# Kernel optimization log

Measured on AMD Instinct MI355X. Metric: run time of the kernel, lower is better.

## Reference

```python
import jax, jax.numpy as jnp
import numpy as np

N_NODES = 50000
N_EDGES = 800000
IN_C, HID_C, OUT_C = 96, 64, 40
ALPHA = 0.2
K = 2
NEG_SLOPE = 0.01  # F.leaky_relu default


def setup_inputs() -> dict:
    key = jax.random.key(0)
    k_x, k_e, k_w0, k_b0, k_w4, k_b4 = jax.random.split(key, 6)
    x = jax.random.normal(k_x, (N_NODES, IN_C), dtype=jnp.float32)
    edge_index = jax.random.randint(k_e, (2, N_EDGES), 0, N_NODES, dtype=jnp.int64)
    # SGConv linear layers (torch.nn.Linear layout: [out, in])
    W0 = jax.random.normal(k_w0, (HID_C, IN_C), dtype=jnp.float32) / np.sqrt(IN_C)
    b0 = jax.random.normal(k_b0, (HID_C,), dtype=jnp.float32) * 0.01
    W4 = jax.random.normal(k_w4, (OUT_C, HID_C), dtype=jnp.float32) / np.sqrt(HID_C)
    b4 = jax.random.normal(k_b4, (OUT_C,), dtype=jnp.float32) * 0.01
    return {"x": x, "edge_index": edge_index, "W0": W0, "b0": b0, "W4": W4, "b4": b4}


def reference(x, edge_index, W0, b0, W4, b4):
    # GCN normalization with self-loops (shared by SGConv and APPNP in PyG):
    # A_hat = A + I, prop(h) = D^{-1/2} A_hat D^{-1/2} h
    n = x.shape[0]
    loops = jnp.arange(n, dtype=edge_index.dtype)
    src = jnp.concatenate([edge_index[0], loops])
    dst = jnp.concatenate([edge_index[1], loops])
    deg = jax.ops.segment_sum(jnp.ones_like(dst, dtype=x.dtype), dst, num_segments=n)
    dinv = jnp.where(deg > 0, jax.lax.rsqrt(deg), 0.0)
    norm = dinv[src] * dinv[dst]  # [E + N]

    def prop(h):
        # gather -> scale -> scatter-add  (irregular memory-bound core op)
        return jax.ops.segment_sum(norm[:, None] * h[src], dst, num_segments=n)

    def sg_prop(h):  # SGConv: K propagation steps, then linear
        for _ in range(K):
            h = prop(h)
        return h

    def appnp(h0):  # APPNP: z_{k+1} = (1-alpha) * prop(z_k) + alpha * h0
        z = h0
        for _ in range(K):
            z = (1.0 - ALPHA) * prop(z) + ALPHA * h0
        return z

    h = sg_prop(x) @ W0.T + b0          # conv0 (SGConv)
    # dropout is identity in eval mode (training=False)
    h = jax.nn.leaky_relu(appnp(h), NEG_SLOPE)   # conv1
    h = jax.nn.leaky_relu(appnp(h), NEG_SLOPE)   # conv2
    h = jax.nn.leaky_relu(appnp(h), NEG_SLOPE)   # conv3
    h = sg_prop(h) @ W4.T + b4          # conv4 (SGConv)
    return jax.nn.log_softmax(h, axis=1)
```

## Files before the change

kernel.cpp:

```cpp
#include <hip/hip_runtime.h>
#include <hip/hip_fp16.h>
#include <math.h>

#define N_NODES 50000
#define N_EDGES 800000
#define IN_C 96
#define HID_C 64
#define OUT_C 40
#define ALPHA 0.2f
#define NEG_SLOPE 0.01f

typedef _Float16 f16x8 __attribute__((ext_vector_type(8)));
typedef float f32x4 __attribute__((ext_vector_type(4)));

__device__ __forceinline__ int edge_at(const void* ei, int is64, long long pos) {
    return is64 ? (int)((const long long*)ei)[pos] : ((const int*)ei)[pos];
}

__global__ void zero_detect_k(int* deg, int n, const unsigned int* ei, int* flag) {
    int i = blockIdx.x * blockDim.x + threadIdx.x;
    if (i < n) deg[i] = 0;
    if (i == 0) {
        int is64 = 1;
        for (int j = 1; j < 16; j += 2)
            if (ei[j] != 0u) is64 = 0;
        *flag = is64;
    }
}

__global__ void deg_hist_k(const void* ei, const int* flag, int* deg, int E) {
    int e = blockIdx.x * blockDim.x + threadIdx.x;
    if (e < E) {
        int d = edge_at(ei, *flag, (long long)E + e);
        atomicAdd(&deg[d], 1);
    }
}

__global__ void scan_p1_k(const int* __restrict__ deg, int* __restrict__ part, int n) {
    __shared__ int sm[256];
    int t = threadIdx.x, i = blockIdx.x * 256 + t;
    int v = (i < n) ? deg[i] : 0;
    sm[t] = v;
    __syncthreads();
    for (int off = 1; off < 256; off <<= 1) {
        int u = (t >= off) ? sm[t - off] : 0;
        __syncthreads();
        sm[t] += u;
        __syncthreads();
    }
    if (t == 255) part[blockIdx.x] = sm[255];
}

__global__ void scan_p2_k(int* part, int nb, int* rowptr, int n) {
    __shared__ int sm[256];
    int t = threadIdx.x;
    int v = (t < nb) ? part[t] : 0;
    sm[t] = v;
    __syncthreads();
    for (int off = 1; off < 256; off <<= 1) {
        int u = (t >= off) ? sm[t - off] : 0;
        __syncthreads();
        sm[t] += u;
        __syncthreads();
    }
    if (t < nb) part[t] = sm[t] - v;
    if (t == 255) rowptr[n] = sm[255];
}

__global__ void scan_p3_k(const int* __restrict__ deg, const int* __restrict__ part,
                          int* __restrict__ rowptr, int* __restrict__ cursor,
                          float* __restrict__ dinv, int n) {
    __shared__ int sm[256];
    int t = threadIdx.x, i = blockIdx.x * 256 + t;
    int v = (i < n) ? deg[i] : 0;
    sm[t] = v;
    __syncthreads();
    for (int off = 1; off < 256; off <<= 1) {
        int u = (t >= off) ? sm[t - off] : 0;
        __syncthreads();
        sm[t] += u;
        __syncthreads();
    }
    if (i < n) {
        int excl = sm[t] - v + part[blockIdx.x];
        rowptr[i] = excl;
        cursor[i] = excl;
        dinv[i] = rsqrtf((float)v + 1.0f);
    }
}

#define FILL_CHUNK 8192
__global__ void csr_fill_k(const void* ei, const int* flag,
                           int* __restrict__ cursor, int* __restrict__ csrc,
                           int E, int N) {
    int p = blockIdx.x & 7;
    int chunk = blockIdx.x >> 3;
    int lo = p * (N / 8), hi = lo + (N / 8);
    int e0 = chunk * FILL_CHUNK;
    int e1 = e0 + FILL_CHUNK; if (e1 > E) e1 = E;
    int f = *flag;
    for (int e = e0 + threadIdx.x; e < e1; e += blockDim.x) {
        int d = edge_at(ei, f, (long long)E + e);
        if (d >= lo && d < hi) {
            int s = edge_at(ei, f, e);
            int pos = atomicAdd(&cursor[d], 1);
            csrc[pos] = s;
        }
    }
}

template <bool COMBINE, bool LEAKY, bool BIAS>
__global__ void prop64_k(const int* __restrict__ rowptr, const int* __restrict__ csrc,
                         const float* __restrict__ dinv,
                         const __half* __restrict__ in, const __half* __restrict__ h0,
                         const float* __restrict__ bias,
                         __half* __restrict__ out, int N) {
    int node = blockIdx.x * (blockDim.x >> 4) + (threadIdx.x >> 4);
    int ci = threadIdx.x & 15;
    if (node >= N) return;
    const float2* in4 = (const float2*)in;
    f32x4 acc;
    {
        float2 r = in4[node * 16 + ci];
        float2 a = __half22float2(*(const __half2*)&r.x);
        float2 b = __half22float2(*(const __half2*)&r.y);
        acc[0] = a.x; acc[1] = a.y; acc[2] = b.x; acc[3] = b.y;
    }
    int r0 = rowptr[node], r1 = rowptr[node + 1];
    int i = r0;
    for (; i + 3 < r1; i += 4) {
        int s0 = csrc[i], s1 = csrc[i + 1], s2 = csrc[i + 2], s3 = csrc[i + 3];
        float2 v0 = in4[s0 * 16 + ci];
        float2 v1 = in4[s1 * 16 + ci];
        float2 v2 = in4[s2 * 16 + ci];
        float2 v3 = in4[s3 * 16 + ci];
        float2 a0 = __half22float2(*(const __half2*)&v0.x), b0 = __half22float2(*(const __half2*)&v0.y);
        float2 a1 = __half22float2(*(const __half2*)&v1.x), b1 = __half22float2(*(const __half2*)&v1.y);
        float2 a2 = __half22float2(*(const __half2*)&v2.x), b2 = __half22float2(*(const __half2*)&v2.y);
        float2 a3 = __half22float2(*(const __half2*)&v3.x), b3 = __half22float2(*(const __half2*)&v3.y);
        acc[0] += (a0.x + a1.x) + (a2.x + a3.x);
        acc[1] += (a0.y + a1.y) + (a2.y + a3.y);
        acc[2] += (b0.x + b1.x) + (b2.x + b3.x);
        acc[3] += (b0.y + b1.y) + (b2.y + b3.y);
    }
    for (; i < r1; ++i) {
        float2 v0 = in4[csrc[i] * 16 + ci];
        float2 a0 = __half22float2(*(const __half2*)&v0.x), b0 = __half22float2(*(const __half2*)&v0.y);
        acc[0] += a0.x; acc[1] += a0.y; acc[2] += b0.x; acc[3] += b0.y;
    }
    float di = dinv[node];
    float sc = di * di;
    float4 v;
    v.x = sc * acc[0]; v.y = sc * acc[1]; v.z = sc * acc[2]; v.w = sc * acc[3];
    if (BIAS) {
        const float4 b = ((const float4*)bias)[ci];
        v.x += di * b.x; v.y += di * b.y; v.z += di * b.z; v.w += di * b.w;
    }
    if (COMBINE) {
        float2 r = ((const float2*)h0)[node * 16 + ci];
        float2 a = __half22float2(*(const __half2*)&r.x);
        float2 b = __half22float2(*(const __half2*)&r.y);
        v.x = (1.0f - ALPHA) * v.x + ALPHA * a.x;
        v.y = (1.0f - ALPHA) * v.y + ALPHA * a.y;
        v.z = (1.0f - ALPHA) * v.z + ALPHA * b.x;
        v.w = (1.0f - ALPHA) * v.w + ALPHA * b.y;
    }
    if (LEAKY) {
        v.x = v.x > 0.0f ? v.x : NEG_SLOPE * v.x;
        v.y = v.y > 0.0f ? v.y : NEG_SLOPE * v.y;
        v.z = v.z > 0.0f ? v.z : NEG_SLOPE * v.z;
        v.w = v.w > 0.0f ? v.w : NEG_SLOPE * v.w;
    }
    float2 o;
    *(__half2*)&o.x = __float22half2_rn(make_float2(v.x, v.y));
    *(__half2*)&o.y = __float22half2_rn(make_float2(v.z, v.w));
    ((float2*)out)[node * 16 + ci] = o;
}

__global__ void prop40_k(const int* __restrict__ rowptr, const int* __restrict__ csrc,
                         const float* __restrict__ dinv,
                         const __half* __restrict__ in, __half* __restrict__ out, int N) {
    constexpr int CP = OUT_C / 2;
    int node = blockIdx.x * (blockDim.x >> 5) + (threadIdx.x >> 5);
    int ci = threadIdx.x & 31;
    if (node >= N) return;
    bool act = ci < CP;
    const __half2* in2 = (const __half2*)in;
    float2 acc = make_float2(0.0f, 0.0f);
    if (act) {
        acc = __half22float2(in2[(long long)node * CP + ci]);
    }
    int r0 = rowptr[node], r1 = rowptr[node + 1];
    int i = r0;
    for (; i + 3 < r1; i += 4) {
        int s0 = csrc[i], s1 = csrc[i + 1], s2 = csrc[i + 2], s3 = csrc[i + 3];
        if (act) {
            float2 v0 = __half22float2(in2[(long long)s0 * CP + ci]);
            float2 v1 = __half22float2(in2[(long long)s1 * CP + ci]);
            float2 v2 = __half22float2(in2[(long long)s2 * CP + ci]);
            float2 v3 = __half22float2(in2[(long long)s3 * CP + ci]);
            acc.x += (v0.x + v1.x) + (v2.x + v3.x);
            acc.y += (v0.y + v1.y) + (v2.y + v3.y);
        }
    }
    for (; i < r1; ++i) {
        int s0 = csrc[i];
        if (act) {
            float2 v0 = __half22float2(in2[(long long)s0 * CP + ci]);
            acc.x += v0.x; acc.y += v0.y;
        }
    }
    if (act) {
        float di = dinv[node];
        float sc = di * di;
        ((__half2*)out)[(long long)node * CP + ci] =
            __float22half2_rn(make_float2(sc * acc.x, sc * acc.y));
    }
}

__global__ void prop40_softmax_k(const int* __restrict__ rowptr, const int* __restrict__ csrc,
                                 const float* __restrict__ dinv,
                                 const __half* __restrict__ in, const float* __restrict__ bias,
                                 float* __restrict__ out, int N) {
    constexpr int CP = OUT_C / 2;
    int node = blockIdx.x * (blockDim.x >> 5) + (threadIdx.x >> 5);
    int ci = threadIdx.x & 31;
    if (node >= N) return;
    bool act = ci < CP;
    const __half2* in2 = (const __half2*)in;
    float2 acc = make_float2(0.0f, 0.0f);
    if (act) {
        acc = __half22float2(in2[(long long)node * CP + ci]);
    }
    int r0 = rowptr[node], r1 = rowptr[node + 1];
    int i = r0;
    for (; i + 3 < r1; i += 4) {
        int s0 = csrc[i], s1 = csrc[i + 1], s2 = csrc[i + 2], s3 = csrc[i + 3];
        if (act) {
            float2 v0 = __half22float2(in2[(long long)s0 * CP + ci]);
            float2 v1 = __half22float2(in2[(long long)s1 * CP + ci]);
            float2 v2 = __half22float2(in2[(long long)s2 * CP + ci]);
            float2 v3 = __half22float2(in2[(long long)s3 * CP + ci]);
            acc.x += (v0.x + v1.x) + (v2.x + v3.x);
            acc.y += (v0.y + v1.y) + (v2.y + v3.y);
        }
    }
    for (; i < r1; ++i) {
        int s0 = csrc[i];
        if (act) {
            float2 v0 = __half22float2(in2[(long long)s0 * CP + ci]);
            acc.x += v0.x; acc.y += v0.y;
        }
    }
    float di = dinv[node];
    float2 v = make_float2(-INFINITY, -INFINITY);
    if (act) {
        v.x = di * acc.x + bias[2 * ci];
        v.y = di * acc.y + bias[2 * ci + 1];
    }
    float m = fmaxf(v.x, v.y);
    #pragma unroll
    for (int off = 16; off >= 1; off >>= 1) m = fmaxf(m, __shfl_xor(m, off));
    float e = act ? (expf(v.x - m) + expf(v.y - m)) : 0.0f;
    #pragma unroll
    for (int off = 16; off >= 1; off >>= 1) e += __shfl_xor(e, off);
    float ls = m + logf(e);
    if (act)
        ((float2*)out)[(long long)node * CP + ci] = make_float2(v.x - ls, v.y - ls);
}

template <int O, int K, bool FP32IN, bool SCALE>
__global__ void __launch_bounds__(256) mfma_lin_k(const void* __restrict__ in_,
                                                  const float* __restrict__ W,
                                                  const float* __restrict__ dinv,
                                                  __half* __restrict__ out, int Mtiles) {
    constexpr int P2 = 52;
    __shared__ __half2 wsh[O * P2];
    for (int idx = threadIdx.x; idx < O * (K / 2); idx += 256) {
        int o = idx / (K / 2), kk = idx - o * (K / 2);
        float2 w2 = ((const float2*)W)[o * (K / 2) + kk];
        wsh[o * P2 + kk] = __floats2half2_rn(w2.x, w2.y);
    }
    __syncthreads();
    int wave = (blockIdx.x * 256 + threadIdx.x) >> 6;
    if (wave >= Mtiles) return;
    int lane = threadIdx.x & 63;
    int lm = lane & 15, q = lane >> 4;
    long long m0 = (long long)wave * 16;
    constexpr int NT = (O + 15) / 16;
    f32x4 acc[NT];
    #pragma unroll
    for (int j = 0; j < NT; ++j) acc[j] = (f32x4){0.f, 0.f, 0.f, 0.f};
    const __half* wsp = (const __half*)wsh;
    #pragma unroll
    for (int k0 = 0; k0 < K; k0 += 32) {
        f16x8 a;
        if (FP32IN) {
            const float* xr = (const float*)in_ + (m0 + lm) * K + k0 + q * 8;
            float4 x0 = ((const float4*)xr)[0];
            float4 x1 = ((const float4*)xr)[1];
            a = (f16x8){(_Float16)x0.x, (_Float16)x0.y, (_Float16)x0.z, (_Float16)x0.w,
                        (_Float16)x1.x, (_Float16)x1.y, (_Float16)x1.z, (_Float16)x1.w};
        } else {
            const __half* xr = (const __half*)in_ + (m0 + lm) * K + k0 + q * 8;
            a = *(const f16x8*)xr;
        }
        #pragma unroll
        for (int j = 0; j < NT; ++j) {
            f16x8 b = *(const f16x8*)(wsp + (16 * j + lm) * (2 * P2) + k0 + q * 8);
            acc[j] = __builtin_amdgcn_mfma_f32_16x16x32_f16(a, b, acc[j], 0, 0, 0);
        }
    }
    #pragma unroll
    for (int r = 0; r < 4; ++r) {
        long long m = m0 + q * 4 + r;
        float sc = SCALE ? dinv[m] : 1.0f;
        #pragma unroll
        for (int j = 0; j < NT; ++j) {
            int col = 16 * j + lm;
            if (col < O) out[m * O + col] = __float2half(acc[j][r] * sc);
        }
    }
}

static inline int cdiv(long long a, long long b) { return (int)((a + b - 1) / b); }
static inline size_t align256(size_t x) { return (x + 255) & ~(size_t)255; }

extern "C" void kernel_launch(void* const* d_in, const int* in_sizes, int n_in,
                              void* d_out, int out_size, void* d_ws, size_t ws_size,
                              hipStream_t stream) {
    const float* x  = (const float*)d_in[0];
    const void*  ei = d_in[1];
    const float* W0 = (const float*)d_in[2];
    const float* b0 = (const float*)d_in[3];
    const float* W4 = (const float*)d_in[4];
    const float* b4 = (const float*)d_in[5];
    float* out = (float*)d_out;

    const int N = N_NODES, E = N_EDGES;
    const int NB = cdiv(N, 256);
    char* ws = (char*)d_ws;
    int*    flag   = (int*)ws;     ws += 256;
    int*    deg    = (int*)ws;     ws += align256((size_t)N * 4);
    int*    rowptr = (int*)ws;     ws += align256((size_t)(N + 1) * 4);
    int*    cursor = (int*)ws;     ws += align256((size_t)N * 4);
    int*    part   = (int*)ws;     ws += align256(256 * 4);
    float*  dinv   = (float*)ws;   ws += align256((size_t)N * 4);
    int*    csrc   = (int*)ws;     ws += align256((size_t)E * 4);
    __half* bufA   = (__half*)ws;  ws += align256((size_t)N * HID_C * 2);
    __half* bufB   = (__half*)ws;  ws += align256((size_t)N * HID_C * 2);
    __half* bufC   = (__half*)ws;  ws += align256((size_t)N * HID_C * 2);

    const int T = 256;
    const int MT = N / 16;
    const int LB = cdiv(MT, 4);
    const int P64B = cdiv(N, T / 16);
    const int P40B = cdiv(N, T / 32);

    zero_detect_k<<<cdiv(N, T), T, 0, stream>>>(deg, N, (const unsigned int*)ei, flag);
    deg_hist_k<<<cdiv(E, T), T, 0, stream>>>(ei, flag, deg, E);
    scan_p1_k<<<NB, 256, 0, stream>>>(deg, part, N);
    scan_p2_k<<<1, 256, 0, stream>>>(part, NB, rowptr, N);
    scan_p3_k<<<NB, 256, 0, stream>>>(deg, part, rowptr, cursor, dinv, N);
    csr_fill_k<<<cdiv(E, FILL_CHUNK) * 8, T, 0, stream>>>(ei, flag, cursor, csrc, E, N);

    mfma_lin_k<HID_C, IN_C, true, true><<<LB, 256, 0, stream>>>(x, W0, dinv, bufA, MT);
    prop64_k<false, false, false><<<P64B, T, 0, stream>>>(
        rowptr, csrc, dinv, bufA, nullptr, nullptr, bufB, N);
    prop64_k<false, false, true><<<P64B, T, 0, stream>>>(
        rowptr, csrc, dinv, bufB, nullptr, b0, bufC, N);

    for (int r = 0; r < 3; ++r) {
        prop64_k<true, false, false><<<P64B, T, 0, stream>>>(
            rowptr, csrc, dinv, bufC, bufC, nullptr, bufB, N);
        prop64_k<true, true, false><<<P64B, T, 0, stream>>>(
            rowptr, csrc, dinv, bufB, bufC, nullptr, bufC, N);
    }

    mfma_lin_k<OUT_C, HID_C, false, false><<<LB, 256, 0, stream>>>(bufC, W4, dinv, bufA, MT);
    prop40_k<<<P40B, T, 0, stream>>>(rowptr, csrc, dinv, bufA, bufB, N);
    prop40_softmax_k<<<P40B, T, 0, stream>>>(rowptr, csrc, dinv, bufB, b4, out, N);
}
```

Baseline: 374.1 us.

## Schedule propagation rows by descending degree via bucketed permutation

```diff
diff --git a/kernel.cpp b/kernel.cpp
--- a/kernel.cpp
+++ b/kernel.cpp
@@ -89,7 +89,53 @@
     }
 }
 
-#define FILL_CHUNK 8192
+__global__ void bhist_k(const int* __restrict__ deg, int* __restrict__ bcnt, int n) {
+    __shared__ int h[64];
+    int t = threadIdx.x, i = blockIdx.x * 256 + t;
+    if (t < 64) h[t] = 0;
+    __syncthreads();
+    if (i < n) {
+        int d = deg[i]; if (d > 63) d = 63;
+        atomicAdd(&h[63 - d], 1);
+    }
+    __syncthreads();
+    if (t < 64) bcnt[blockIdx.x * 64 + t] = h[t];
+}
+
+__global__ void bscan_k(const int* __restrict__ bcnt, int* __restrict__ bbase, int nb) {
+    __shared__ int tot[64];
+    int b = threadIdx.x;
+    int s = 0;
+    for (int j = 0; j < nb; ++j) s += bcnt[j * 64 + b];
+    tot[b] = s;
+    __syncthreads();
+    if (b == 0) {
+        int run = 0;
+        for (int k = 0; k < 64; ++k) { int v = tot[k]; tot[k] = run; run += v; }
+    }
+    __syncthreads();
+    int run = tot[b];
+    for (int j = 0; j < nb; ++j) {
+        bbase[j * 64 + b] = run;
+        run += bcnt[j * 64 + b];
+    }
+}
+
+__global__ void perm_k(const int* __restrict__ deg, const int* __restrict__ bbase,
+                       int* __restrict__ perm, int n) {
+    __shared__ int h[64];
+    int t = threadIdx.x, i = blockIdx.x * 256 + t;
+    if (t < 64) h[t] = 0;
+    __syncthreads();
+    if (i < n) {
+        int d = deg[i]; if (d > 63) d = 63;
+        int b = 63 - d;
+        int rank = atomicAdd(&h[b], 1);
+        perm[bbase[blockIdx.x * 64 + b] + rank] = i;
+    }
+}
+
+#define FILL_CHUNK 2048
 __global__ void csr_fill_k(const void* ei, const int* flag,
                            int* __restrict__ cursor, int* __restrict__ csrc,
                            int E, int N) {
@@ -99,25 +145,34 @@
     int e0 = chunk * FILL_CHUNK;
     int e1 = e0 + FILL_CHUNK; if (e1 > E) e1 = E;
     int f = *flag;
-    for (int e = e0 + threadIdx.x; e < e1; e += blockDim.x) {
-        int d = edge_at(ei, f, (long long)E + e);
-        if (d >= lo && d < hi) {
+    for (int e = e0 + threadIdx.x; e < e1; e += 2 * blockDim.x) {
+        int e2 = e + blockDim.x;
+        int d0 = edge_at(ei, f, (long long)E + e);
+        int d1 = (e2 < e1) ? edge_at(ei, f, (long long)E + e2) : -1;
+        if (d0 >= lo && d0 < hi) {
             int s = edge_at(ei, f, e);
-            int pos = atomicAdd(&cursor[d], 1);
+            int pos = atomicAdd(&cursor[d0], 1);
             csrc[pos] = s;
         }
+        if (d1 >= lo && d1 < hi) {
+            int s = edge_at(ei, f, e2);
+            int pos = atomicAdd(&cursor[d1], 1);
+            csrc[pos] = s;
+        }
     }
 }
 
 template <bool COMBINE, bool LEAKY, bool BIAS>
-__global__ void prop64_k(const int* __restrict__ rowptr, const int* __restrict__ csrc,
+__global__ void prop64_k(const int* __restrict__ perm,
+                         const int* __restrict__ rowptr, const int* __restrict__ csrc,
                          const float* __restrict__ dinv,
                          const __half* __restrict__ in, const __half* __restrict__ h0,
                          const float* __restrict__ bias,
                          __half* __restrict__ out, int N) {
-    int node = blockIdx.x * (blockDim.x >> 4) + (threadIdx.x >> 4);
+    int qw = blockIdx.x * (blockDim.x >> 4) + (threadIdx.x >> 4);
     int ci = threadIdx.x & 15;
-    if (node >= N) return;
+    if (qw >= N) return;
+    int node = perm[qw];
     const float2* in4 = (const float2*)in;
     f32x4 acc;
     {
@@ -177,13 +232,15 @@
     ((float2*)out)[node * 16 + ci] = o;
 }
 
-__global__ void prop40_k(const int* __restrict__ rowptr, const int* __restrict__ csrc,
+__global__ void prop40_k(const int* __restrict__ perm,
+                         const int* __restrict__ rowptr, const int* __restrict__ csrc,
                          const float* __restrict__ dinv,
                          const __half* __restrict__ in, __half* __restrict__ out, int N) {
     constexpr int CP = OUT_C / 2;
-    int node = blockIdx.x * (blockDim.x >> 5) + (threadIdx.x >> 5);
+    int hw = blockIdx.x * (blockDim.x >> 5) + (threadIdx.x >> 5);
     int ci = threadIdx.x & 31;
-    if (node >= N) return;
+    if (hw >= N) return;
+    int node = perm[hw];
     bool act = ci < CP;
     const __half2* in2 = (const __half2*)in;
     float2 acc = make_float2(0.0f, 0.0f);
@@ -218,14 +275,16 @@
     }
 }
 
-__global__ void prop40_softmax_k(const int* __restrict__ rowptr, const int* __restrict__ csrc,
+__global__ void prop40_softmax_k(const int* __restrict__ perm,
+                                 const int* __restrict__ rowptr, const int* __restrict__ csrc,
                                  const float* __restrict__ dinv,
                                  const __half* __restrict__ in, const float* __restrict__ bias,
                                  float* __restrict__ out, int N) {
     constexpr int CP = OUT_C / 2;
-    int node = blockIdx.x * (blockDim.x >> 5) + (threadIdx.x >> 5);
+    int hw = blockIdx.x * (blockDim.x >> 5) + (threadIdx.x >> 5);
     int ci = threadIdx.x & 31;
-    if (node >= N) return;
+    if (hw >= N) return;
+    int node = perm[hw];
     bool act = ci < CP;
     const __half2* in2 = (const __half2*)in;
     float2 acc = make_float2(0.0f, 0.0f);
@@ -345,6 +404,9 @@
     int*    rowptr = (int*)ws;     ws += align256((size_t)(N + 1) * 4);
     int*    cursor = (int*)ws;     ws += align256((size_t)N * 4);
     int*    part   = (int*)ws;     ws += align256(256 * 4);
+    int*    bcnt   = (int*)ws;     ws += align256((size_t)NB * 64 * 4);
+    int*    bbase  = (int*)ws;     ws += align256((size_t)NB * 64 * 4);
+    int*    perm   = (int*)ws;     ws += align256((size_t)N * 4);
     float*  dinv   = (float*)ws;   ws += align256((size_t)N * 4);
     int*    csrc   = (int*)ws;     ws += align256((size_t)E * 4);
     __half* bufA   = (__half*)ws;  ws += align256((size_t)N * HID_C * 2);
@@ -362,22 +424,25 @@
     scan_p1_k<<<NB, 256, 0, stream>>>(deg, part, N);
     scan_p2_k<<<1, 256, 0, stream>>>(part, NB, rowptr, N);
     scan_p3_k<<<NB, 256, 0, stream>>>(deg, part, rowptr, cursor, dinv, N);
+    bhist_k<<<NB, 256, 0, stream>>>(deg, bcnt, N);
+    bscan_k<<<1, 64, 0, stream>>>(bcnt, bbase, NB);
+    perm_k<<<NB, 256, 0, stream>>>(deg, bbase, perm, N);
     csr_fill_k<<<cdiv(E, FILL_CHUNK) * 8, T, 0, stream>>>(ei, flag, cursor, csrc, E, N);
 
     mfma_lin_k<HID_C, IN_C, true, true><<<LB, 256, 0, stream>>>(x, W0, dinv, bufA, MT);
     prop64_k<false, false, false><<<P64B, T, 0, stream>>>(
-        rowptr, csrc, dinv, bufA, nullptr, nullptr, bufB, N);
+        perm, rowptr, csrc, dinv, bufA, nullptr, nullptr, bufB, N);
     prop64_k<false, false, true><<<P64B, T, 0, stream>>>(
-        rowptr, csrc, dinv, bufB, nullptr, b0, bufC, N);
+        perm, rowptr, csrc, dinv, bufB, nullptr, b0, bufC, N);
 
     for (int r = 0; r < 3; ++r) {
         prop64_k<true, false, false><<<P64B, T, 0, stream>>>(
-            rowptr, csrc, dinv, bufC, bufC, nullptr, bufB, N);
+            perm, rowptr, csrc, dinv, bufC, bufC, nullptr, bufB, N);
         prop64_k<true, true, false><<<P64B, T, 0, stream>>>(
-            rowptr, csrc, dinv, bufB, bufC, nullptr, bufC, N);
+            perm, rowptr, csrc, dinv, bufB, bufC, nullptr, bufC, N);
     }
 
     mfma_lin_k<OUT_C, HID_C, false, false><<<LB, 256, 0, stream>>>(bufC, W4, dinv, bufA, MT);
-    prop40_k<<<P40B, T, 0, stream>>>(rowptr, csrc, dinv, bufA, bufB, N);
-    prop40_softmax_k<<<P40B, T, 0, stream>>>(rowptr, csrc, dinv, bufB, b4, out, N);
-}
+    prop40_k<<<P40B, T, 0, stream>>>(perm, rowptr, csrc, dinv, bufA, bufB, N);
+    prop40_softmax_k<<<P40B, T, 0, stream>>>(perm, rowptr, csrc, dinv, bufB, b4, out, N);
+}
```

New measurement: 393.2 us. 5.1% more time.
